# Performance work log

Measured on AMD Instinct MI355X. Metric: run time of the kernel, lower is better.

Reference implementation:

```python
import jax, jax.numpy as jnp
import numpy as np


def setup_inputs() -> dict:
    key = jax.random.key(0)
    ks = jax.random.split(key, 5)
    T, B, C, H, K = 2048, 8, 1024, 16, 7
    s = 1.0 / np.sqrt(C)
    return {
        "x": jax.random.normal(ks[0], (T, B, C), dtype=jnp.float32),
        "w_weight": jax.random.normal(ks[1], (H * K, C), dtype=jnp.float32) * s,
        "glu_w": jax.random.normal(ks[2], (2 * H, C), dtype=jnp.float32) * s,
        "glu_b": jnp.zeros((2 * H,), dtype=jnp.float32),
        "out_w": jax.random.normal(ks[3], (C, C), dtype=jnp.float32) * s,
        "out_b": jnp.zeros((C,), dtype=jnp.float32),
        "padding_l": 6,
    }


def reference(x, w_weight, glu_w, glu_b, out_w, out_b, padding_l):
    # x: (T, B, C) in TBC format
    T, B, C = x.shape
    H = glu_w.shape[0] // 2
    K = w_weight.shape[0] // H
    R = C // H  # channels per head

    # GLU gate: C -> 2H, split last dim, a * sigmoid(b)  -> (T, B, H)
    g = (x @ glu_w.T + glu_b).reshape(T, B, H, 2)
    gate = g[..., 0] * jax.nn.sigmoid(g[..., 1])

    # per-position per-head kernel weights, softmax over K -> (T, B, H, K)
    w = jax.nn.softmax((x @ w_weight.T).reshape(T, B, H, K), axis=-1)

    # depthwise dynamic conv: out[t] = sum_k w[t,k] * x_pad[t + k]
    xh = x.reshape(T, B, H, R)
    xp = jnp.pad(xh, ((padding_l, K - 1 - padding_l), (0, 0), (0, 0), (0, 0)))
    conv = jnp.zeros_like(xh)
    for k in range(K):  # K is small & static; avoids (B,H,T,K,R) unfold blowup
        conv = conv + w[..., k:k + 1] * jax.lax.dynamic_slice_in_dim(xp, k, T, axis=0)

    # gate per head, merge heads, output projection
    out = (conv * gate[..., None]).reshape(T, B, C)
    return out @ out_w.T + out_b
```

## Files before the change

kernel.cpp:

```cpp
#include <hip/hip_runtime.h>
#include <hip/hip_bf16.h>
#include <stdint.h>

#define T_DIM 2048
#define B_DIM 8
#define C_DIM 1024
#define H_DIM 16
#define K_DIM 7
#define M_DIM (T_DIM * B_DIM)
#define NLOG 144
#define CW_STRIDE 128

typedef __attribute__((ext_vector_type(8))) short short8;
typedef __attribute__((ext_vector_type(4))) float floatx4;

__device__ __forceinline__ ushort f2bf(float f) {
    __hip_bfloat16 h = __float2bfloat16(f);
    return *(ushort*)&h;
}

#define S_W  ((size_t)112 * C_DIM)
#define S_G  ((size_t)32 * C_DIM)
#define S_O  ((size_t)C_DIM * C_DIM)
#define S_WG (S_W + S_G)
#define S_CVT (S_WG + S_O)

__global__ __launch_bounds__(256) void cvt_w_kernel(
    const float* __restrict__ w_weight, const float* __restrict__ glu_w,
    const float* __restrict__ out_w,
    ushort* __restrict__ wb, ushort* __restrict__ Wb)
{
    size_t gid = ((size_t)blockIdx.x * 256 + threadIdx.x) * 4;
    const float* src; ushort* dst; size_t off;
    if (gid < S_W)            { src = w_weight; dst = wb;       off = gid; }
    else if (gid < S_WG)      { src = glu_w;    dst = wb + S_W; off = gid - S_W; }
    else                      { src = out_w;    dst = Wb;       off = gid - S_WG; }
    float4 v = *(const float4*)(src + off);
    ushort4 o; o.x = f2bf(v.x); o.y = f2bf(v.y); o.z = f2bf(v.z); o.w = f2bf(v.w);
    *(ushort4*)(dst + off) = o;
}

__global__ __launch_bounds__(256) void logits_kernel(
    const float* __restrict__ x,
    const ushort* __restrict__ wb,
    const float* __restrict__ glu_b,
    float* __restrict__ cw)
{
    __shared__ __align__(16) ushort Bs[2][144 * 32];
    __shared__ float lsm[64][NLOG];

    const int tid = threadIdx.x;
    const int wave = tid >> 6, lane = tid & 63;
    const int fr = lane & 15, q = lane >> 4;
    const int m0 = blockIdx.x * 64;
    const int mrow = m0 + wave * 16 + fr;

    floatx4 acc[9];
#pragma unroll
    for (int j = 0; j < 9; ++j) acc[j] = (floatx4){0.f, 0.f, 0.f, 0.f};

    const float* arow = x + (size_t)mrow * C_DIM + q * 8;

    for (int i = tid; i < 576; i += 256) {
        int r = i >> 2, ch = i & 3;
        __builtin_amdgcn_global_load_lds(
            (const __attribute__((address_space(1))) void*)(wb + (size_t)r * C_DIM + ch * 8),
            (__attribute__((address_space(3))) void*)(&Bs[0][0] + i * 8), 16, 0, 0);
    }
    float4 a0 = *(const float4*)(arow);
    float4 a1 = *(const float4*)(arow + 4);
    __syncthreads();

    for (int kc = 0; kc < 32; ++kc) {
        const int buf = kc & 1;
        if (kc < 31) {
            const ushort* wsrc = wb + (kc + 1) * 32;
            for (int i = tid; i < 576; i += 256) {
                int r = i >> 2, ch = i & 3;
                __builtin_amdgcn_global_load_lds(
                    (const __attribute__((address_space(1))) void*)(wsrc + (size_t)r * C_DIM + ch * 8),
                    (__attribute__((address_space(3))) void*)(&Bs[buf ^ 1][0] + i * 8), 16, 0, 0);
            }
        }
        short8 a;
        a[0] = (short)f2bf(a0.x); a[1] = (short)f2bf(a0.y);
        a[2] = (short)f2bf(a0.z); a[3] = (short)f2bf(a0.w);
        a[4] = (short)f2bf(a1.x); a[5] = (short)f2bf(a1.y);
        a[6] = (short)f2bf(a1.z); a[7] = (short)f2bf(a1.w);
        if (kc < 31) {
            a0 = *(const float4*)(arow + (kc + 1) * 32);
            a1 = *(const float4*)(arow + (kc + 1) * 32 + 4);
        }
#pragma unroll
        for (int j = 0; j < 9; ++j) {
            short8 b = *(const short8*)(&Bs[buf][0] + ((j * 16 + fr) * 4 + q) * 8);
            acc[j] = __builtin_amdgcn_mfma_f32_16x16x32_bf16(a, b, acc[j], 0, 0, 0);
        }
        __syncthreads();
    }

#pragma unroll
    for (int j = 0; j < 9; ++j)
#pragma unroll
        for (int r = 0; r < 4; ++r)
            lsm[wave * 16 + q * 4 + r][j * 16 + fr] = acc[j][r];
    __syncthreads();

    {
        const int row = tid >> 2;
        const int hbase = (tid & 3) * 4;
        float* crow = cw + (size_t)(m0 + row) * CW_STRIDE;
#pragma unroll
        for (int hh = 0; hh < 4; ++hh) {
            const int h = hbase + hh;
            float l[K_DIM];
            float mx = -1e30f;
#pragma unroll
            for (int k = 0; k < K_DIM; ++k) { l[k] = lsm[row][h * K_DIM + k]; mx = fmaxf(mx, l[k]); }
            float s = 0.f;
#pragma unroll
            for (int k = 0; k < K_DIM; ++k) { l[k] = __expf(l[k] - mx); s += l[k]; }
            float inv = 1.f / s;
#pragma unroll
            for (int k = 0; k < K_DIM; ++k) crow[h * K_DIM + k] = l[k] * inv;
            float ga = lsm[row][112 + 2 * h] + glu_b[2 * h];
            float gb = lsm[row][113 + 2 * h] + glu_b[2 * h + 1];
            crow[112 + h] = ga * (1.f / (1.f + __expf(-gb)));
        }
    }
}

__global__ __launch_bounds__(256) void conv_kernel(
    const float* __restrict__ x,
    const float* __restrict__ cw,
    const int* __restrict__ padding_l_,
    ushort* __restrict__ y)
{
    const int lb = (blockIdx.x & 7) * 512 + (blockIdx.x >> 3);
    const int wave = threadIdx.x >> 6, lane = threadIdx.x & 63;
    const int m = lb * 4 + wave;
    const int t = m >> 3;
    const int pad = *padding_l_;
    const int h = lane >> 2;

    const float* crow = cw + (size_t)m * CW_STRIDE;
    float wt[K_DIM];
#pragma unroll
    for (int k = 0; k < K_DIM; ++k) wt[k] = crow[h * K_DIM + k];
    const float g = crow[112 + h];

    const int c0 = lane * 16;
    float av[16];
#pragma unroll
    for (int i = 0; i < 16; ++i) av[i] = 0.f;

#pragma unroll
    for (int k = 0; k < K_DIM; ++k) {
        int ts = t + k - pad;
        if (ts < 0 || ts >= T_DIM) continue;
        float wv = wt[k];
        const float4* xp = (const float4*)(x + ((size_t)m + 8 * (k - pad)) * C_DIM + c0);
        float4 u0 = xp[0], u1 = xp[1], u2 = xp[2], u3 = xp[3];
        av[0]  += wv * u0.x; av[1]  += wv * u0.y; av[2]  += wv * u0.z; av[3]  += wv * u0.w;
        av[4]  += wv * u1.x; av[5]  += wv * u1.y; av[6]  += wv * u1.z; av[7]  += wv * u1.w;
        av[8]  += wv * u2.x; av[9]  += wv * u2.y; av[10] += wv * u2.z; av[11] += wv * u2.w;
        av[12] += wv * u3.x; av[13] += wv * u3.y; av[14] += wv * u3.z; av[15] += wv * u3.w;
    }

    uint32_t o[8];
#pragma unroll
    for (int i = 0; i < 8; ++i)
        o[i] = (uint32_t)f2bf(av[2 * i] * g) | ((uint32_t)f2bf(av[2 * i + 1] * g) << 16);
    uint4* yr = (uint4*)(y + (size_t)m * C_DIM + c0);
    yr[0] = (uint4){o[0], o[1], o[2], o[3]};
    yr[1] = (uint4){o[4], o[5], o[6], o[7]};
}

__global__ __launch_bounds__(512, 2) void out_gemm(
    const ushort* __restrict__ y,
    const ushort* __restrict__ Wb,
    const float* __restrict__ bias,
    float* __restrict__ out)
{
    __shared__ __align__(16) ushort SM[2][4][128 * 64];

    const int orig = (blockIdx.x & 7) * 32 + (blockIdx.x >> 3);
    const int bm = orig >> 2;
    const int bn = orig & 3;
    const int m0 = bm * 256, n0 = bn * 256;
    const int tid = threadIdx.x;
    const int lane = tid & 63, wave = tid >> 6;
    const int wr = wave >> 2;
    const int wc = wave & 3;
    const int fr = lane & 15, q = lane >> 4;
    const int g0 = ((q) ^ (fr & 7)) * 8;
    const int g1 = ((4 + q) ^ (fr & 7)) * 8;

    floatx4 acc[8][4];
#pragma unroll
    for (int i = 0; i < 8; ++i)
#pragma unroll
        for (int j = 0; j < 4; ++j) acc[i][j] = (floatx4){0.f, 0.f, 0.f, 0.f};

    auto stageH = [&](int buf, int mat, int half, int k0) {
        const ushort* src = mat ? Wb : y;
        const int row0 = (mat ? n0 : m0) + half * 128;
        ushort* dst = &SM[buf][mat * 2 + half][0];
#pragma unroll
        for (int j = 0; j < 2; ++j) {
            int idx = j * 512 + tid;
            int r = idx >> 3, gl = idx & 7;
            int gs = gl ^ (r & 7);
            __builtin_amdgcn_global_load_lds(
                (const __attribute__((address_space(1))) void*)(src + (size_t)(row0 + r) * C_DIM + k0 + gs * 8),
                (__attribute__((address_space(3))) void*)(dst + idx * 8), 16, 0, 0);
        }
    };

    stageH(0, 0, 0, 0);  stageH(0, 0, 1, 0);
    stageH(0, 1, 0, 0);  stageH(0, 1, 1, 0);
    stageH(1, 1, 0, 64); stageH(1, 1, 1, 64);
    asm volatile("s_waitcnt vmcnt(4)" ::: "memory");
    __builtin_amdgcn_s_barrier();
    asm volatile("" ::: "memory");

    short8 a[4][2], b[4][2];
    for (int t = 0; t < 16; ++t) {
        const int buf = t & 1;
        const ushort* Ar = &SM[buf][wr][0];
        const ushort* Br = &SM[buf][2 + (wc >> 1)][0];
        const int brb = (wc & 1) * 64;

#pragma unroll
        for (int mf = 0; mf < 4; ++mf) {
            int ro = (mf * 16 + fr) * 64;
            a[mf][0] = *(const short8*)(Ar + ro + g0);
            a[mf][1] = *(const short8*)(Ar + ro + g1);
        }
#pragma unroll
        for (int nf = 0; nf < 2; ++nf) {
            int ro = (brb + nf * 16 + fr) * 64;
            b[nf][0] = *(const short8*)(Br + ro + g0);
            b[nf][1] = *(const short8*)(Br + ro + g1);
        }
        if (t + 1 < 16) stageH(buf ^ 1, 0, 0, (t + 1) * 64);
        __builtin_amdgcn_s_barrier();
        asm volatile("s_waitcnt lgkmcnt(0)" ::: "memory");
        __builtin_amdgcn_s_setprio(1);
#pragma unroll
        for (int ks = 0; ks < 2; ++ks)
#pragma unroll
            for (int mf = 0; mf < 4; ++mf)
#pragma unroll
                for (int nf = 0; nf < 2; ++nf)
                    acc[mf][nf] = __builtin_amdgcn_mfma_f32_16x16x32_bf16(a[mf][ks], b[nf][ks], acc[mf][nf], 0, 0, 0);
        __builtin_amdgcn_s_setprio(0);
        asm volatile("" ::: "memory");
        __builtin_amdgcn_s_barrier();
        asm volatile("" ::: "memory");

#pragma unroll
        for (int nf = 2; nf < 4; ++nf) {
            int ro = (brb + nf * 16 + fr) * 64;
            b[nf][0] = *(const short8*)(Br + ro + g0);
            b[nf][1] = *(const short8*)(Br + ro + g1);
        }
        if (t + 1 < 16) stageH(buf ^ 1, 0, 1, (t + 1) * 64);
        __builtin_amdgcn_s_barrier();
        asm volatile("s_waitcnt lgkmcnt(0)" ::: "memory");
        __builtin_amdgcn_s_setprio(1);
#pragma unroll
        for (int ks = 0; ks < 2; ++ks)
#pragma unroll
            for (int mf = 0; mf < 4; ++mf)
#pragma unroll
                for (int nf = 2; nf < 4; ++nf)
                    acc[mf][nf] = __builtin_amdgcn_mfma_f32_16x16x32_bf16(a[mf][ks], b[nf][ks], acc[mf][nf], 0, 0, 0);
        __builtin_amdgcn_s_setprio(0);
        asm volatile("" ::: "memory");
        __builtin_amdgcn_s_barrier();
        asm volatile("" ::: "memory");

#pragma unroll
        for (int mf = 0; mf < 4; ++mf) {
            int ro = ((mf + 4) * 16 + fr) * 64;
            a[mf][0] = *(const short8*)(Ar + ro + g0);
            a[mf][1] = *(const short8*)(Ar + ro + g1);
        }
        if (t + 2 < 16) stageH(buf, 1, 0, (t + 2) * 64);
        __builtin_amdgcn_s_barrier();
        asm volatile("s_waitcnt lgkmcnt(0)" ::: "memory");
        __builtin_amdgcn_s_setprio(1);
#pragma unroll
        for (int ks = 0; ks < 2; ++ks)
#pragma unroll
            for (int mf = 0; mf < 4; ++mf)
#pragma unroll
                for (int nf = 0; nf < 2; ++nf)
                    acc[mf + 4][nf] = __builtin_amdgcn_mfma_f32_16x16x32_bf16(a[mf][ks], b[nf][ks], acc[mf + 4][nf], 0, 0, 0);
        __builtin_amdgcn_s_setprio(0);
        asm volatile("" ::: "memory");
        __builtin_amdgcn_s_barrier();
        asm volatile("" ::: "memory");

        if (t + 2 < 16) stageH(buf, 1, 1, (t + 2) * 64);
        if (t < 14)       { asm volatile("s_waitcnt vmcnt(4)" ::: "memory"); }
        else if (t == 14) { asm volatile("s_waitcnt vmcnt(0)" ::: "memory"); }
        __builtin_amdgcn_s_barrier();
        asm volatile("" ::: "memory");
        __builtin_amdgcn_s_setprio(1);
#pragma unroll
        for (int ks = 0; ks < 2; ++ks)
#pragma unroll
            for (int mf = 0; mf < 4; ++mf)
#pragma unroll
                for (int nf = 2; nf < 4; ++nf)
                    acc[mf + 4][nf] = __builtin_amdgcn_mfma_f32_16x16x32_bf16(a[mf][ks], b[nf][ks], acc[mf + 4][nf], 0, 0, 0);
        __builtin_amdgcn_s_setprio(0);
        asm volatile("" ::: "memory");
        __builtin_amdgcn_s_barrier();
        asm volatile("" ::: "memory");
    }

#pragma unroll
    for (int nf = 0; nf < 4; ++nf) {
        int n = n0 + wc * 64 + nf * 16 + fr;
        float bv = bias[n];
#pragma unroll
        for (int mf = 0; mf < 8; ++mf) {
#pragma unroll
            for (int r = 0; r < 4; ++r) {
                int m = m0 + wr * 128 + mf * 16 + q * 4 + r;
                out[(size_t)m * C_DIM + n] = acc[mf][nf][r] + bv;
            }
        }
    }
}

extern "C" void kernel_launch(void* const* d_in, const int* in_sizes, int n_in,
                              void* d_out, int out_size, void* d_ws, size_t ws_size,
                              hipStream_t stream) {
    const float* x        = (const float*)d_in[0];
    const float* w_weight = (const float*)d_in[1];
    const float* glu_w    = (const float*)d_in[2];
    const float* glu_b    = (const float*)d_in[3];
    const float* out_w    = (const float*)d_in[4];
    const float* out_b    = (const float*)d_in[5];
    const int* padding_l  = (const int*)d_in[6];
    float* out = (float*)d_out;

    char* ws = (char*)d_ws;
    ushort* y  = (ushort*)ws;
    ushort* wb = y + (size_t)M_DIM * C_DIM;
    ushort* Wb = wb + S_WG;
    float* cwp = (float*)(Wb + S_O);

    cvt_w_kernel<<<S_CVT / 4 / 256, 256, 0, stream>>>(w_weight, glu_w, out_w, wb, Wb);
    logits_kernel<<<M_DIM / 64, 256, 0, stream>>>(x, wb, glu_b, cwp);
    conv_kernel<<<M_DIM / 4, 256, 0, stream>>>(x, cwp, padding_l, y);
    out_gemm<<<(M_DIM / 256) * (C_DIM / 256), 512, 0, stream>>>(y, Wb, out_b, out);
}
```

Baseline: 216.5 us.

## Split logits GEMM K across two wave groups and read weights directly

The logits kernel now launches 512 threads per block: two groups of four waves each compute half of the K=1024 reduction, and the partial results are summed through shared memory. The LDS double-buffered staging of the bf16 weights and its per-iteration barriers are removed, so each lane loads its B fragments straight from global memory (the weights are small and likely L2-resident). This is meant to remove the synchronization stalls and raise per-block parallelism. In exchange it adds redundant global weight traffic and an extra shared-memory reduction step, and the lsm stride is padded to 146.

```diff
diff --git a/kernel.cpp b/kernel.cpp
--- a/kernel.cpp
+++ b/kernel.cpp
@@ -10,6 +10,7 @@
 #define M_DIM (T_DIM * B_DIM)
 #define NLOG 144
 #define CW_STRIDE 128
+#define LSM_STRIDE 146
 
 typedef __attribute__((ext_vector_type(8))) short short8;
 typedef __attribute__((ext_vector_type(4))) float floatx4;
@@ -40,78 +41,74 @@
     *(ushort4*)(dst + off) = o;
 }
 
-__global__ __launch_bounds__(256) void logits_kernel(
+__global__ __launch_bounds__(512) void logits_kernel(
     const float* __restrict__ x,
     const ushort* __restrict__ wb,
     const float* __restrict__ glu_b,
     float* __restrict__ cw)
 {
-    __shared__ __align__(16) ushort Bs[2][144 * 32];
-    __shared__ float lsm[64][NLOG];
+    __shared__ float lsm[64][LSM_STRIDE];
 
     const int tid = threadIdx.x;
     const int wave = tid >> 6, lane = tid & 63;
+    const int g = wave & 3;
+    const int kh = wave >> 2;
     const int fr = lane & 15, q = lane >> 4;
     const int m0 = blockIdx.x * 64;
-    const int mrow = m0 + wave * 16 + fr;
+    const int mrow = m0 + g * 16 + fr;
+    const int kb = kh * 512;
 
     floatx4 acc[9];
 #pragma unroll
     for (int j = 0; j < 9; ++j) acc[j] = (floatx4){0.f, 0.f, 0.f, 0.f};
 
-    const float* arow = x + (size_t)mrow * C_DIM + q * 8;
-
-    for (int i = tid; i < 576; i += 256) {
-        int r = i >> 2, ch = i & 3;
-        __builtin_amdgcn_global_load_lds(
-            (const __attribute__((address_space(1))) void*)(wb + (size_t)r * C_DIM + ch * 8),
-            (__attribute__((address_space(3))) void*)(&Bs[0][0] + i * 8), 16, 0, 0);
-    }
+    const float* arow = x + (size_t)mrow * C_DIM + kb + q * 8;
+    const ushort* brow = wb + (size_t)fr * C_DIM + kb + q * 8;
+
     float4 a0 = *(const float4*)(arow);
     float4 a1 = *(const float4*)(arow + 4);
-    __syncthreads();
-
-    for (int kc = 0; kc < 32; ++kc) {
-        const int buf = kc & 1;
-        if (kc < 31) {
-            const ushort* wsrc = wb + (kc + 1) * 32;
-            for (int i = tid; i < 576; i += 256) {
-                int r = i >> 2, ch = i & 3;
-                __builtin_amdgcn_global_load_lds(
-                    (const __attribute__((address_space(1))) void*)(wsrc + (size_t)r * C_DIM + ch * 8),
-                    (__attribute__((address_space(3))) void*)(&Bs[buf ^ 1][0] + i * 8), 16, 0, 0);
-            }
-        }
+
+#pragma unroll 2
+    for (int kc = 0; kc < 16; ++kc) {
         short8 a;
         a[0] = (short)f2bf(a0.x); a[1] = (short)f2bf(a0.y);
         a[2] = (short)f2bf(a0.z); a[3] = (short)f2bf(a0.w);
         a[4] = (short)f2bf(a1.x); a[5] = (short)f2bf(a1.y);
         a[6] = (short)f2bf(a1.z); a[7] = (short)f2bf(a1.w);
-        if (kc < 31) {
+        if (kc < 15) {
             a0 = *(const float4*)(arow + (kc + 1) * 32);
             a1 = *(const float4*)(arow + (kc + 1) * 32 + 4);
         }
 #pragma unroll
         for (int j = 0; j < 9; ++j) {
-            short8 b = *(const short8*)(&Bs[buf][0] + ((j * 16 + fr) * 4 + q) * 8);
+            short8 b = *(const short8*)(brow + (size_t)j * 16 * C_DIM + kc * 32);
             acc[j] = __builtin_amdgcn_mfma_f32_16x16x32_bf16(a, b, acc[j], 0, 0, 0);
         }
-        __syncthreads();
-    }
-
-#pragma unroll
-    for (int j = 0; j < 9; ++j)
-#pragma unroll
-        for (int r = 0; r < 4; ++r)
-            lsm[wave * 16 + q * 4 + r][j * 16 + fr] = acc[j][r];
+    }
+
+    if (kh == 0) {
+#pragma unroll
+        for (int j = 0; j < 9; ++j)
+#pragma unroll
+            for (int r = 0; r < 4; ++r)
+                lsm[g * 16 + q * 4 + r][j * 16 + fr] = acc[j][r];
+    }
     __syncthreads();
+    if (kh == 1) {
+#pragma unroll
+        for (int j = 0; j < 9; ++j)
+#pragma unroll
+            for (int r = 0; r < 4; ++r)
+                lsm[g * 16 + q * 4 + r][j * 16 + fr] += acc[j][r];
+    }
+    __syncthreads();
 
     {
-        const int row = tid >> 2;
-        const int hbase = (tid & 3) * 4;
+        const int row = tid >> 3;
+        const int hbase = (tid & 7) * 2;
         float* crow = cw + (size_t)(m0 + row) * CW_STRIDE;
 #pragma unroll
-        for (int hh = 0; hh < 4; ++hh) {
+        for (int hh = 0; hh < 2; ++hh) {
             const int h = hbase + hh;
             float l[K_DIM];
             float mx = -1e30f;
@@ -356,7 +353,7 @@
     float* cwp = (float*)(Wb + S_O);
 
     cvt_w_kernel<<<S_CVT / 4 / 256, 256, 0, stream>>>(w_weight, glu_w, out_w, wb, Wb);
-    logits_kernel<<<M_DIM / 64, 256, 0, stream>>>(x, wb, glu_b, cwp);
+    logits_kernel<<<M_DIM / 64, 512, 0, stream>>>(x, wb, glu_b, cwp);
     conv_kernel<<<M_DIM / 4, 256, 0, stream>>>(x, cwp, padding_l, y);
     out_gemm<<<(M_DIM / 256) * (C_DIM / 256), 512, 0, stream>>>(y, Wb, out_b, out);
 }
```

Result: no change. 218.3 us (+0.8%).
